# Kernel tuning notes

Hardware: AMD Instinct MI355X
Metric: run time of the kernel (lower is better)

The kernel has to match this reference:

```python
import jax, jax.numpy as jnp
import numpy as np
from jax import lax

_CLIP_MIN = 1e-06
_CLIP_MAX = 1.0
_POS_ALPHA = 0.0005
NUM_CLASSES = 21
RADIUS = 3
HALF_D = RADIUS * RADIUS
POOL = 3
PAD = POOL // 2
IGNORE = 255
LAM = 0.5  # loss_weight_lambda, lambda_way=1


def _max_pool(x):
    # NCHW max pool, kernel=stride=3, padding=1
    return lax.reduce_window(x, -jnp.inf, lax.max,
                             (1, 1, POOL, POOL), (1, 1, POOL, POOL),
                             ((0, 0), (0, 0), (PAD, PAD), (PAD, PAD)))


def _get_pairs(x):
    # stack radius*radius shifted crops -> [N, C, r^2, nh, nw]
    h, w = x.shape[2], x.shape[3]
    nh, nw = h - RADIUS + 1, w - RADIUS + 1
    crops = [x[:, :, y:y + nh, xo:xo + nw] for y in range(RADIUS) for xo in range(RADIUS)]
    return jnp.stack(crops, axis=2)


def _log_det_by_cholesky(m):
    chol = jnp.linalg.cholesky(m)
    return 2.0 * jnp.sum(jnp.log(jnp.diagonal(chol, axis1=-2, axis2=-1) + 1e-08), axis=-1)


def _rmi_lower_bound(labels_4d, probs_4d):
    la = _max_pool(labels_4d)
    pr = _max_pool(probs_4d)
    n, c = la.shape[0], la.shape[1]
    la_v = _get_pairs(la).reshape(n, c, HALF_D, -1)   # [N,C,d,L]
    pr_v = _get_pairs(pr).reshape(n, c, HALF_D, -1)
    la_v = la_v - jnp.mean(la_v, axis=3, keepdims=True)
    pr_v = pr_v - jnp.mean(pr_v, axis=3, keepdims=True)
    la_cov = jnp.einsum('ncdl,ncel->ncde', la_v, la_v)
    pr_cov = jnp.einsum('ncdl,ncel->ncde', pr_v, pr_v)
    eye = jnp.eye(HALF_D, dtype=la_cov.dtype)
    pr_cov_inv = jnp.linalg.inv(pr_cov + eye * _POS_ALPHA)
    la_pr_cov = jnp.einsum('ncdl,ncel->ncde', la_v, pr_v)
    appro_var = la_cov - jnp.einsum('ncde,ncef,ncgf->ncdg', la_pr_cov, pr_cov_inv, la_pr_cov)
    rmi_now = 0.5 * _log_det_by_cholesky(appro_var + eye * _POS_ALPHA)  # [N,C]
    rmi_per_class = jnp.mean(rmi_now.reshape(-1, NUM_CLASSES), axis=0) / float(HALF_D)
    return jnp.sum(rmi_per_class)


def setup_inputs() -> dict:
    key = jax.random.key(0)
    k1, k2 = jax.random.split(key)
    score = jax.random.normal(k1, (4, NUM_CLASSES, 512, 512), dtype=jnp.float32)
    target = jax.random.randint(k2, (4, 512, 512), 0, NUM_CLASSES, dtype=jnp.int64)
    return {"score": score, "target": target}


def reference(score, target):
    # cross entropy with ignore_index=255, mean reduction
    logp = jax.nn.log_softmax(score, axis=1)                      # [N,C,H,W]
    valid_ce = (target != IGNORE)
    safe_t = jnp.where(valid_ce, target, 0)
    nll = -jnp.take_along_axis(logp, safe_t[:, None].astype(jnp.int32), axis=1)[:, 0]
    normal_loss = jnp.sum(jnp.where(valid_ce, nll, 0.0)) / jnp.sum(valid_ce.astype(jnp.float32))

    # valid one-hot labels and masked sigmoid probs
    mask = (target < NUM_CLASSES)                                 # [N,H,W]
    maskf = mask.astype(jnp.float32)
    onehot = jax.nn.one_hot((target * mask).astype(jnp.int32), NUM_CLASSES, dtype=jnp.float32)
    onehot = onehot * maskf[..., None]                            # [N,H,W,C]
    onehot = jnp.transpose(onehot, (0, 3, 1, 2))                  # [N,C,H,W]
    probs = jnp.clip(jax.nn.sigmoid(score) * maskf[:, None], _CLIP_MIN, _CLIP_MAX)

    rmi_loss = _rmi_lower_bound(onehot, probs)
    return LAM * normal_loss + rmi_loss * (1.0 - LAM)
```

## Files before the change

kernel.cpp:

```cpp
#include <hip/hip_runtime.h>
#include <cfloat>
#include <cmath>

#define DEVINL __device__ __forceinline__

constexpr int N_ = 4, C_ = 21, H_ = 512, W_ = 512;
constexpr int P_ = 171;
constexpr int Q_ = 169;
constexpr int NC_ = N_ * C_;
constexpr int HW_ = H_ * W_;
constexpr int PROW_ = 172;
constexpr int PPAD_ = PROW_ * P_;
constexpr int NCOV_ = 189;
constexpr float EPS_ = 5e-4f;
constexpr int RC_ = 29;
constexpr int G_ = 43;

DEVINL constexpr int tstart(int d) { return d * 9 - d * (d - 1) / 2; }

DEVINL float wave_sum(float v) {
#pragma unroll
    for (int o = 32; o > 0; o >>= 1) v += __shfl_down(v, o, 64);
    return v;
}

__global__ __launch_bounds__(256) void k_fused(const float* __restrict__ score,
                                               const int* __restrict__ target,
                                               float* __restrict__ pr,
                                               float* __restrict__ la,
                                               float* __restrict__ cov) {
    __shared__ unsigned sh_pack[86];
    __shared__ float rn[4], rc[4];
    int half = blockIdx.x;
    int i = blockIdx.y;
    int n = blockIdx.z;
    int t = threadIdx.x;
    int c0 = half * 256;
    int jlo = half * 86;
    int ncell = half ? 85 : 86;

    float nll = 0.f, cnt = 0.f;
    {
        int r = t >> 6, q = t & 63;
        int rowbase = (i == 0) ? 0 : 3 * i - 1;
        int nrows = (i == 0) ? 2 : 3;
        if (r < nrows) {
            int row = rowbase + r;
            size_t pixoff = (size_t)row * W_ + c0 + 4 * q;
            const float* sp = score + (size_t)n * C_ * HW_ + pixoff;
            float4 s[C_];
#pragma unroll
            for (int c = 0; c < C_; ++c)
                s[c] = *(const float4*)(sp + (size_t)c * HW_);
            int4 t4 = *(const int4*)(target + (size_t)n * HW_ + pixoff);

            float4 se = {0.f, 0.f, 0.f, 0.f};
            float4 stgt = {0.f, 0.f, 0.f, 0.f};
#pragma unroll
            for (int c = 0; c < C_; ++c) {
                se.x += __expf(s[c].x);
                se.y += __expf(s[c].y);
                se.z += __expf(s[c].z);
                se.w += __expf(s[c].w);
                if (t4.x == c) stgt.x = s[c].x;
                if (t4.y == c) stgt.y = s[c].y;
                if (t4.z == c) stgt.z = s[c].z;
                if (t4.w == c) stgt.w = s[c].w;
            }
            if (t4.x != 255) { nll += __logf(se.x) - stgt.x; cnt += 1.f; }
            if (t4.y != 255) { nll += __logf(se.y) - stgt.y; cnt += 1.f; }
            if (t4.z != 255) { nll += __logf(se.z) - stgt.z; cnt += 1.f; }
            if (t4.w != 255) { nll += __logf(se.w) - stgt.w; cnt += 1.f; }
        }
    }
    nll = wave_sum(nll);
    cnt = wave_sum(cnt);
    {
        int wv = t >> 6, lane = t & 63;
        if (lane == 0) { rn[wv] = nll; rc[wv] = cnt; }
    }

    if (t < ncell) {
        int j = jlo + t;
        int hl = 3 * i - 1; if (hl < 0) hl = 0;
        int wl = 3 * j - 1; if (wl < 0) wl = 0;
        int hmax = 3 * i + 1, wmax = 3 * j + 1;
        const int* tb = target + (size_t)n * HW_;
        unsigned oh = 0, px = 0;
#pragma unroll
        for (int r = 0; r < 3; ++r) {
            int hh = hl + r;
            bool hv = hh <= hmax;
            const int* trow = tb + hh * W_;
#pragma unroll
            for (int dc = 0; dc < 3; ++dc) {
                int ww = wl + dc;
                int tv = trow[ww];
                if (hv && (ww <= wmax) && tv >= 0 && tv < C_) {
                    oh |= 1u << tv;
                    px |= 1u << (r * 3 + dc);
                }
            }
        }
        sh_pack[t] = oh | (px << 23);
    }
    __syncthreads();

    if (t == 0)
        atomicAdd(&cov[NC_ * NCOV_ + 0], rn[0] + rn[1] + rn[2] + rn[3]);
    if (t == 64)
        atomicAdd(&cov[NC_ * NCOV_ + 1], rc[0] + rc[1] + rc[2] + rc[3]);

    int hl = 3 * i - 1; if (hl < 0) hl = 0;
    for (int item = t; item < C_ * 86; item += 256) {
        int c = item / 86;
        int jj = item - c * 86;
        if (jj >= ncell) continue;
        int j = jlo + jj;
        int wl = 3 * j - 1; if (wl < 0) wl = 0;
        int ncidx = n * C_ + c;
        const float* sp = score + (size_t)ncidx * HW_ + (size_t)hl * W_ + wl;
        unsigned pk = sh_pack[jj];
        unsigned px = pk >> 23;
        float vm = -FLT_MAX;
#pragma unroll
        for (int r = 0; r < 3; ++r) {
#pragma unroll
            for (int dc = 0; dc < 3; ++dc) {
                float v = sp[r * W_ + dc];
                vm = fmaxf(vm, ((px >> (r * 3 + dc)) & 1u) ? v : -FLT_MAX);
            }
        }
        float p = __builtin_amdgcn_rcpf(1.f + __expf(-vm));
        p = fminf(fmaxf(p, 1e-6f), 1.f);
        size_t ob = (size_t)ncidx * PPAD_ + (size_t)i * PROW_ + j;
        pr[ob] = p;
        la[ob] = ((pk >> c) & 1u) ? 1.f : 0.f;
    }
}

template <bool WITH_S1, int D0, int D1>
DEVINL void cov_tri(const float* __restrict__ X, float* __restrict__ cov,
                    int nc, int r0, int rend, int s1base, int s2base,
                    int tid, float (*red)[33]) {
    constexpr int NS2 = ((9 - D0) * (10 - D0) - (9 - D1) * (10 - D1)) / 2;
    constexpr int RLO = D0 / 3;
    constexpr int NS1 = WITH_S1 ? 9 : 0;
    constexpr int KOFF = tstart(D0);
    float s1[9], s2[NS2];
#pragma unroll
    for (int k = 0; k < 9; ++k) s1[k] = 0.f;
#pragma unroll
    for (int k = 0; k < NS2; ++k) s2[k] = 0.f;

    int nitems = (rend - r0) * G_;
    for (int idx = tid; idx < nitems; idx += 256) {
        int lr = idx / G_;
        int q = idx - lr * G_;
        int x0 = q * 4;
        const float* base = X + (size_t)(r0 + lr) * PROW_ + x0;
        float v[3][8];
#pragma unroll
        for (int r = RLO; r < 3; ++r) {
            float4 u0 = *(const float4*)(base + r * PROW_);
            float4 u1 = *(const float4*)(base + r * PROW_ + 4);
            v[r][0] = u0.x; v[r][1] = u0.y; v[r][2] = u0.z; v[r][3] = u0.w;
            v[r][4] = u1.x; v[r][5] = u1.y; v[r][6] = u1.z; v[r][7] = u1.w;
        }
#pragma unroll
        for (int p = 0; p < 4; ++p) {
            if (x0 + p < Q_) {
                if constexpr (WITH_S1) {
#pragma unroll
                    for (int d = 0; d < 9; ++d) s1[d] += v[d / 3][p + d % 3];
                }
                int k = 0;
#pragma unroll
                for (int d = D0; d < D1; ++d)
#pragma unroll
                    for (int e = d; e < 9; ++e) {
                        s2[k] += v[d / 3][p + d % 3] * v[e / 3][p + e % 3];
                        ++k;
                    }
            }
        }
    }

    int lane = tid & 63, wv = tid >> 6;
    if constexpr (WITH_S1) {
#pragma unroll
        for (int k = 0; k < 9; ++k) { float v2 = wave_sum(s1[k]); if (lane == 0) red[wv][k] = v2; }
    }
#pragma unroll
    for (int k = 0; k < NS2; ++k) { float v2 = wave_sum(s2[k]); if (lane == 0) red[wv][NS1 + k] = v2; }
    __syncthreads();
    for (int k = tid; k < NS1 + NS2; k += 256) {
        float v2 = red[0][k] + red[1][k] + red[2][k] + red[3][k];
        int dst = (WITH_S1 && k < 9) ? (s1base + k) : (s2base + KOFF + k - NS1);
        atomicAdd(&cov[nc * NCOV_ + dst], v2);
    }
}

template <int RA>
DEVINL void cov_ab(const float* __restrict__ A, const float* __restrict__ B,
                   float* __restrict__ cov, int nc, int r0, int rend,
                   int tid, float (*red)[33]) {
    float sab[27];
#pragma unroll
    for (int k = 0; k < 27; ++k) sab[k] = 0.f;

    int nitems = (rend - r0) * G_;
    for (int idx = tid; idx < nitems; idx += 256) {
        int lr = idx / G_;
        int q = idx - lr * G_;
        int x0 = q * 4;
        size_t off = (size_t)(r0 + lr) * PROW_ + x0;
        float a[8], b[3][8];
        {
            float4 u0 = *(const float4*)(A + off + RA * PROW_);
            float4 u1 = *(const float4*)(A + off + RA * PROW_ + 4);
            a[0] = u0.x; a[1] = u0.y; a[2] = u0.z; a[3] = u0.w;
            a[4] = u1.x; a[5] = u1.y; a[6] = u1.z; a[7] = u1.w;
        }
#pragma unroll
        for (int r = 0; r < 3; ++r) {
            float4 w0 = *(const float4*)(B + off + r * PROW_);
            float4 w1 = *(const float4*)(B + off + r * PROW_ + 4);
            b[r][0] = w0.x; b[r][1] = w0.y; b[r][2] = w0.z; b[r][3] = w0.w;
            b[r][4] = w1.x; b[r][5] = w1.y; b[r][6] = w1.z; b[r][7] = w1.w;
        }
#pragma unroll
        for (int p = 0; p < 4; ++p) {
            if (x0 + p < Q_) {
#pragma unroll
                for (int dm = 0; dm < 3; ++dm)
#pragma unroll
                    for (int e = 0; e < 9; ++e)
                        sab[dm * 9 + e] += a[p + dm] * b[e / 3][p + e % 3];
            }
        }
    }

    int lane = tid & 63, wv = tid >> 6;
#pragma unroll
    for (int k = 0; k < 27; ++k) { float v2 = wave_sum(sab[k]); if (lane == 0) red[wv][k] = v2; }
    __syncthreads();
    for (int k = tid; k < 27; k += 256) {
        float v2 = red[0][k] + red[1][k] + red[2][k] + red[3][k];
        atomicAdd(&cov[nc * NCOV_ + 108 + RA * 27 + k], v2);
    }
}

__global__ __launch_bounds__(256) void k_cov(const float* __restrict__ la,
                                             const float* __restrict__ pr,
                                             float* __restrict__ cov) {
    __shared__ float red[4][33];
    int nc = blockIdx.x;
    int chunk = blockIdx.y;
    int part = blockIdx.z;
    int r0 = chunk * RC_;
    int rend = r0 + RC_;
    if (rend > Q_) rend = Q_;
    int tid = threadIdx.x;
    const float* LA = la + (size_t)nc * PPAD_;
    const float* PR = pr + (size_t)nc * PPAD_;

    switch (part) {
        case 0: cov_tri<true, 0, 3>(LA, cov, nc, r0, rend, 0, 18, tid, red); break;
        case 1: cov_tri<false, 3, 9>(LA, cov, nc, r0, rend, 0, 18, tid, red); break;
        case 2: cov_tri<true, 0, 3>(PR, cov, nc, r0, rend, 9, 63, tid, red); break;
        case 3: cov_tri<false, 3, 9>(PR, cov, nc, r0, rend, 9, 63, tid, red); break;
        case 4: cov_ab<0>(LA, PR, cov, nc, r0, rend, tid, red); break;
        case 5: cov_ab<1>(LA, PR, cov, nc, r0, rend, tid, red); break;
        case 6: cov_ab<2>(LA, PR, cov, nc, r0, rend, tid, red); break;
    }
}

__global__ __launch_bounds__(128) void k_final(const float* __restrict__ cov,
                                               float* __restrict__ out) {
    __shared__ float red[128];
    int t = threadIdx.x;
    float my = 0.f;
    if (t < NC_) {
        const float* S = cov + t * NCOV_;
        const float Lf = (float)(Q_ * Q_);
        float sA[9], sB[9];
#pragma unroll
        for (int d = 0; d < 9; ++d) { sA[d] = S[d]; sB[d] = S[9 + d]; }
        float laC[45], M[45], Cm[81];
        {
            int k = 0;
#pragma unroll
            for (int d = 0; d < 9; ++d)
#pragma unroll
                for (int e = d; e < 9; ++e) {
                    laC[k] = S[18 + k] - sA[d] * sA[e] / Lf;
                    M[k] = S[63 + k] - sB[d] * sB[e] / Lf + (d == e ? EPS_ : 0.f);
                    ++k;
                }
#pragma unroll
            for (int d = 0; d < 9; ++d)
#pragma unroll
                for (int e = 0; e < 9; ++e)
                    Cm[d * 9 + e] = S[108 + d * 9 + e] - sA[d] * sB[e] / Lf;
        }
#pragma unroll
        for (int j = 0; j < 9; ++j) {
            float s = M[tstart(j)];
#pragma unroll
            for (int k = 0; k < j; ++k) { float l = M[tstart(k) + (j - k)]; s -= l * l; }
            float dj = sqrtf(fmaxf(s, 1e-30f));
            M[tstart(j)] = dj;
            float inv = 1.f / dj;
#pragma unroll
            for (int i = j + 1; i < 9; ++i) {
                float s2 = M[tstart(j) + (i - j)];
#pragma unroll
                for (int k = 0; k < j; ++k)
                    s2 -= M[tstart(k) + (i - k)] * M[tstart(k) + (j - k)];
                M[tstart(j) + (i - j)] = s2 * inv;
            }
        }
#pragma unroll
        for (int p = 0; p < 9; ++p) {
#pragma unroll
            for (int i = 0; i < 9; ++i) {
                float s = Cm[p * 9 + i];
#pragma unroll
                for (int k = 0; k < i; ++k)
                    s -= M[tstart(k) + (i - k)] * Cm[p * 9 + k];
                Cm[p * 9 + i] = s / M[tstart(i)];
            }
        }
#pragma unroll
        for (int d = 0; d < 9; ++d)
#pragma unroll
            for (int e = d; e < 9; ++e) {
                float s = 0.f;
#pragma unroll
                for (int i = 0; i < 9; ++i) s += Cm[d * 9 + i] * Cm[e * 9 + i];
                laC[tstart(d) + (e - d)] -= s;
                if (d == e) laC[tstart(d)] += EPS_;
            }
        float rmi = 0.f;
#pragma unroll
        for (int j = 0; j < 9; ++j) {
            float s = laC[tstart(j)];
#pragma unroll
            for (int k = 0; k < j; ++k) { float l = laC[tstart(k) + (j - k)]; s -= l * l; }
            float dj = sqrtf(fmaxf(s, 0.f));
            laC[tstart(j)] = dj;
            float inv = 1.f / fmaxf(dj, 1e-30f);
#pragma unroll
            for (int i = j + 1; i < 9; ++i) {
                float s2 = laC[tstart(j) + (i - j)];
#pragma unroll
                for (int k = 0; k < j; ++k)
                    s2 -= laC[tstart(k) + (i - k)] * laC[tstart(k) + (j - k)];
                laC[tstart(j) + (i - j)] = s2 * inv;
            }
            rmi += __logf(dj + 1e-8f);
        }
        my = rmi;
    }
    red[t] = my;
    __syncthreads();
#pragma unroll
    for (int o = 64; o > 0; o >>= 1) {
        if (t < o) red[t] += red[t + o];
        __syncthreads();
    }
    if (t == 0) {
        float rmi_total = red[0] / 36.f;
        float ce = cov[NC_ * NCOV_ + 0] / cov[NC_ * NCOV_ + 1];
        out[0] = 0.5f * ce + 0.5f * rmi_total;
    }
}

extern "C" void kernel_launch(void* const* d_in, const int* in_sizes, int n_in,
                              void* d_out, int out_size, void* d_ws, size_t ws_size,
                              hipStream_t stream) {
    const float* score = (const float*)d_in[0];
    const int* target = (const int*)d_in[1];
    float* pr = (float*)d_ws;
    float* la = pr + (size_t)NC_ * PPAD_;
    float* cov = la + (size_t)NC_ * PPAD_;
    hipMemsetAsync(cov, 0, (size_t)(NC_ * NCOV_ + 2) * sizeof(float), stream);

    k_fused<<<dim3(2, P_, N_), dim3(256), 0, stream>>>(score, target, pr, la, cov);
    k_cov<<<dim3(NC_, 6, 7), dim3(256), 0, stream>>>(la, pr, cov);
    k_final<<<dim3(1), dim3(128), 0, stream>>>(cov, (float*)d_out);
}
```

Baseline: 246.6 us.

## Vectorize pooled sigmoid loads into 4-cell groups and split CE/packing across waves

The pooling stage now has each work item handle a group of four output cells. It loads 3x16 floats with float4 vector loads instead of nine scalar loads per cell. Cross-entropy runs on waves 0-2 with score channels loaded in batches of seven to limit register pressure, while wave 3 builds the shared one-hot/pixel masks concurrently. This aims to cut memory instructions and raise load efficiency, at the cost of more register usage, changed cell partitioning across the two blocks, and more complex edge handling.

After: 246.9 us. Within noise of the previous version (+0.1%).

```diff
diff --git a/kernel.cpp b/kernel.cpp
--- a/kernel.cpp
+++ b/kernel.cpp
@@ -24,118 +24,148 @@
     return v;
 }
 
+template <int IDX>
+DEVINL void do_cell(const float (&f)[3][16], unsigned pk, int c, float* prp, float* lap) {
+    unsigned px = pk >> 23;
+    float vm = -FLT_MAX;
+#pragma unroll
+    for (int r = 0; r < 3; ++r)
+#pragma unroll
+        for (int dc = 0; dc < 3; ++dc)
+            vm = fmaxf(vm, ((px >> (r * 3 + dc)) & 1u) ? f[r][IDX + dc] : -FLT_MAX);
+    float p = __builtin_amdgcn_rcpf(1.f + __expf(-vm));
+    p = fminf(fmaxf(p, 1e-6f), 1.f);
+    *prp = p;
+    *lap = ((pk >> c) & 1u) ? 1.f : 0.f;
+}
+
 __global__ __launch_bounds__(256) void k_fused(const float* __restrict__ score,
                                                const int* __restrict__ target,
                                                float* __restrict__ pr,
                                                float* __restrict__ la,
                                                float* __restrict__ cov) {
-    __shared__ unsigned sh_pack[86];
+    __shared__ unsigned sh_pack[88];
     __shared__ float rn[4], rc[4];
     int half = blockIdx.x;
     int i = blockIdx.y;
     int n = blockIdx.z;
     int t = threadIdx.x;
+    int wv = t >> 6, lane = t & 63;
     int c0 = half * 256;
-    int jlo = half * 86;
-    int ncell = half ? 85 : 86;
+    int jlo = half ? 88 : 0;
+    int ncell = half ? 83 : 88;
+    int glo = half ? 22 : 0;
+    int gn = half ? 21 : 22;
+
+    int hl = 3 * i - 1; if (hl < 0) hl = 0;
+    int rowbase = (i == 0) ? 0 : 3 * i - 1;
+    int nrows = (i == 0) ? 2 : 3;
 
     float nll = 0.f, cnt = 0.f;
-    {
-        int r = t >> 6, q = t & 63;
-        int rowbase = (i == 0) ? 0 : 3 * i - 1;
-        int nrows = (i == 0) ? 2 : 3;
-        if (r < nrows) {
-            int row = rowbase + r;
-            size_t pixoff = (size_t)row * W_ + c0 + 4 * q;
+    if (wv < 3) {
+        if (wv < nrows) {
+            int row = rowbase + wv;
+            size_t pixoff = (size_t)row * W_ + c0 + 4 * lane;
             const float* sp = score + (size_t)n * C_ * HW_ + pixoff;
-            float4 s[C_];
-#pragma unroll
-            for (int c = 0; c < C_; ++c)
-                s[c] = *(const float4*)(sp + (size_t)c * HW_);
             int4 t4 = *(const int4*)(target + (size_t)n * HW_ + pixoff);
 
             float4 se = {0.f, 0.f, 0.f, 0.f};
             float4 stgt = {0.f, 0.f, 0.f, 0.f};
-#pragma unroll
-            for (int c = 0; c < C_; ++c) {
-                se.x += __expf(s[c].x);
-                se.y += __expf(s[c].y);
-                se.z += __expf(s[c].z);
-                se.w += __expf(s[c].w);
-                if (t4.x == c) stgt.x = s[c].x;
-                if (t4.y == c) stgt.y = s[c].y;
-                if (t4.z == c) stgt.z = s[c].z;
-                if (t4.w == c) stgt.w = s[c].w;
+            float4 s[7];
+#pragma unroll
+            for (int cb = 0; cb < C_; cb += 7) {
+#pragma unroll
+                for (int u = 0; u < 7; ++u)
+                    s[u] = *(const float4*)(sp + (size_t)(cb + u) * HW_);
+                asm volatile("" ::: "memory");
+#pragma unroll
+                for (int u = 0; u < 7; ++u) {
+                    int c = cb + u;
+                    se.x += __expf(s[u].x);
+                    se.y += __expf(s[u].y);
+                    se.z += __expf(s[u].z);
+                    se.w += __expf(s[u].w);
+                    if (t4.x == c) stgt.x = s[u].x;
+                    if (t4.y == c) stgt.y = s[u].y;
+                    if (t4.z == c) stgt.z = s[u].z;
+                    if (t4.w == c) stgt.w = s[u].w;
+                }
             }
             if (t4.x != 255) { nll += __logf(se.x) - stgt.x; cnt += 1.f; }
             if (t4.y != 255) { nll += __logf(se.y) - stgt.y; cnt += 1.f; }
             if (t4.z != 255) { nll += __logf(se.z) - stgt.z; cnt += 1.f; }
             if (t4.w != 255) { nll += __logf(se.w) - stgt.w; cnt += 1.f; }
         }
+    } else {
+        for (int idx = lane; idx < ncell; idx += 64) {
+            int j = jlo + idx;
+            int wl = 3 * j - 1; if (wl < 0) wl = 0;
+            int hmax = 3 * i + 1, wmax = 3 * j + 1;
+            const int* tb = target + (size_t)n * HW_;
+            unsigned oh = 0, px = 0;
+#pragma unroll
+            for (int r = 0; r < 3; ++r) {
+                int hh = hl + r;
+                bool hv = hh <= hmax;
+                const int* trow = tb + hh * W_;
+#pragma unroll
+                for (int dc = 0; dc < 3; ++dc) {
+                    int ww = wl + dc;
+                    int tv = trow[ww];
+                    if (hv && (ww <= wmax) && tv >= 0 && tv < C_) {
+                        oh |= 1u << tv;
+                        px |= 1u << (r * 3 + dc);
+                    }
+                }
+            }
+            sh_pack[idx] = oh | (px << 23);
+        }
     }
     nll = wave_sum(nll);
     cnt = wave_sum(cnt);
-    {
-        int wv = t >> 6, lane = t & 63;
-        if (lane == 0) { rn[wv] = nll; rc[wv] = cnt; }
-    }
-
-    if (t < ncell) {
-        int j = jlo + t;
-        int hl = 3 * i - 1; if (hl < 0) hl = 0;
-        int wl = 3 * j - 1; if (wl < 0) wl = 0;
-        int hmax = 3 * i + 1, wmax = 3 * j + 1;
-        const int* tb = target + (size_t)n * HW_;
-        unsigned oh = 0, px = 0;
-#pragma unroll
-        for (int r = 0; r < 3; ++r) {
-            int hh = hl + r;
-            bool hv = hh <= hmax;
-            const int* trow = tb + hh * W_;
-#pragma unroll
-            for (int dc = 0; dc < 3; ++dc) {
-                int ww = wl + dc;
-                int tv = trow[ww];
-                if (hv && (ww <= wmax) && tv >= 0 && tv < C_) {
-                    oh |= 1u << tv;
-                    px |= 1u << (r * 3 + dc);
-                }
-            }
-        }
-        sh_pack[t] = oh | (px << 23);
-    }
+    if (lane == 0) { rn[wv] = nll; rc[wv] = cnt; }
     __syncthreads();
-
     if (t == 0)
         atomicAdd(&cov[NC_ * NCOV_ + 0], rn[0] + rn[1] + rn[2] + rn[3]);
     if (t == 64)
         atomicAdd(&cov[NC_ * NCOV_ + 1], rc[0] + rc[1] + rc[2] + rc[3]);
 
-    int hl = 3 * i - 1; if (hl < 0) hl = 0;
-    for (int item = t; item < C_ * 86; item += 256) {
-        int c = item / 86;
-        int jj = item - c * 86;
-        if (jj >= ncell) continue;
-        int j = jlo + jj;
-        int wl = 3 * j - 1; if (wl < 0) wl = 0;
+    int nitems = C_ * gn;
+    for (int it = t; it < nitems; it += 256) {
+        int c = it / gn;
+        int gg = it - c * gn;
+        int g = glo + gg;
+        int b = (g == 0) ? 0 : 12 * g - 4;
+        int o3 = (b + 15 < W_) ? 12 : 8;
         int ncidx = n * C_ + c;
-        const float* sp = score + (size_t)ncidx * HW_ + (size_t)hl * W_ + wl;
-        unsigned pk = sh_pack[jj];
-        unsigned px = pk >> 23;
-        float vm = -FLT_MAX;
+        const float* sb = score + (size_t)ncidx * HW_ + (size_t)hl * W_ + b;
+        float f[3][16];
 #pragma unroll
         for (int r = 0; r < 3; ++r) {
-#pragma unroll
-            for (int dc = 0; dc < 3; ++dc) {
-                float v = sp[r * W_ + dc];
-                vm = fmaxf(vm, ((px >> (r * 3 + dc)) & 1u) ? v : -FLT_MAX);
-            }
-        }
-        float p = __builtin_amdgcn_rcpf(1.f + __expf(-vm));
-        p = fminf(fmaxf(p, 1e-6f), 1.f);
-        size_t ob = (size_t)ncidx * PPAD_ + (size_t)i * PROW_ + j;
-        pr[ob] = p;
-        la[ob] = ((pk >> c) & 1u) ? 1.f : 0.f;
+            const float* rp = sb + r * W_;
+            float4 q0 = *(const float4*)(rp);
+            float4 q1 = *(const float4*)(rp + 4);
+            float4 q2 = *(const float4*)(rp + 8);
+            float4 q3 = *(const float4*)(rp + o3);
+            f[r][0] = q0.x;  f[r][1] = q0.y;  f[r][2] = q0.z;  f[r][3] = q0.w;
+            f[r][4] = q1.x;  f[r][5] = q1.y;  f[r][6] = q1.z;  f[r][7] = q1.w;
+            f[r][8] = q2.x;  f[r][9] = q2.y;  f[r][10] = q2.z; f[r][11] = q2.w;
+            f[r][12] = q3.x; f[r][13] = q3.y; f[r][14] = q3.z; f[r][15] = q3.w;
+        }
+        int sb0 = 4 * g - jlo;
+        size_t ob = (size_t)ncidx * PPAD_ + (size_t)i * PROW_ + 4 * g;
+        if (g == 0) {
+            do_cell<0>(f, sh_pack[sb0 + 0], c, pr + ob + 0, la + ob + 0);
+            do_cell<2>(f, sh_pack[sb0 + 1], c, pr + ob + 1, la + ob + 1);
+            do_cell<5>(f, sh_pack[sb0 + 2], c, pr + ob + 2, la + ob + 2);
+            do_cell<8>(f, sh_pack[sb0 + 3], c, pr + ob + 3, la + ob + 3);
+        } else {
+            do_cell<3>(f, sh_pack[sb0 + 0], c, pr + ob + 0, la + ob + 0);
+            do_cell<6>(f, sh_pack[sb0 + 1], c, pr + ob + 1, la + ob + 1);
+            do_cell<9>(f, sh_pack[sb0 + 2], c, pr + ob + 2, la + ob + 2);
+            if (4 * g + 3 < P_)
+                do_cell<12>(f, sh_pack[sb0 + 3], c, pr + ob + 3, la + ob + 3);
+        }
     }
 }
 
```
